# Kernel tuning notes

Measured on AMD Instinct MI355X. Metric: run time of the kernel, lower is better.

Reference implementation:

```python
import jax, jax.numpy as jnp
import numpy as np

B, X, Y, Z = 2, 64, 64, 48
T_IN, T_OUT = 10, 20
WIDTH = 20
G = 4              # number of fields / groups
M1 = M2 = M3 = 8   # fourier modes
L = 4              # layers
ORDER = [[0, 1, 2, 3], [1, 2, 3, 0], [2, 3, 0, 1], [3, 0, 1, 2]]
CIN = WIDTH * 4    # mWidth_input_parameters[i] == 4
COUT = WIDTH       # nWidth_output_parameters[i] == 1
EPS = 1e-5


def setup_inputs() -> dict:
    key = jax.random.key(0)
    ks = jax.random.split(key, 12)
    s = 0.02
    return {
        "x": jax.random.normal(ks[0], (B, X, Y, Z, G * T_IN), jnp.float32),
        "p_w": jax.random.normal(ks[1], (G, T_IN + 3, WIDTH), jnp.float32) * s,
        "p_b": jnp.zeros((G, WIDTH), jnp.float32),
        # complex spectral weights stored as (..., 2) = (real, imag); 4 corner blocks
        "spec_w": jax.random.normal(ks[2], (L, G, 4, CIN, COUT, M1, M2, M3, 2), jnp.float32) * (1.0 / CIN),
        "mlp_w1": jax.random.normal(ks[3], (L, G, COUT, COUT), jnp.float32) * s,
        "mlp_b1": jnp.zeros((L, G, COUT), jnp.float32),
        "mlp_w2": jax.random.normal(ks[4], (L, G, COUT, COUT), jnp.float32) * s,
        "mlp_b2": jnp.zeros((L, G, COUT), jnp.float32),
        "w_w": jax.random.normal(ks[5], (L, G, COUT, CIN), jnp.float32) * s,
        "w_b": jnp.zeros((L, G, COUT), jnp.float32),
        "q_w1": jax.random.normal(ks[6], (G, 4 * COUT, COUT), jnp.float32) * s,
        "q_b1": jnp.zeros((G, 4 * COUT), jnp.float32),
        "q_w2": jax.random.normal(ks[7], (G, T_OUT, 4 * COUT), jnp.float32) * s,
        "q_b2": jnp.zeros((G, T_OUT), jnp.float32),
    }


def _instance_norm(v):  # (B,C,X,Y,Z); InstanceNorm3d, affine=False
    m = v.mean(axis=(-3, -2, -1), keepdims=True)
    var = v.var(axis=(-3, -2, -1), keepdims=True)
    return (v - m) * jax.lax.rsqrt(var + EPS)


def _conv1x1(v, w, b):  # w: (Co, Ci)
    return jnp.einsum('bixyz,oi->boxyz', v, w) + b[None, :, None, None, None]


def _gelu(v):
    return jax.nn.gelu(v, approximate=False)


def _spectral(v, w):  # v: (B,Ci,X,Y,Z); w: complex (4,Ci,Co,M1,M2,M3)
    ft = jnp.fft.rfftn(v, axes=(-3, -2, -1))
    mul = lambda xc, wc: jnp.einsum('bixyz,ioxyz->boxyz', xc, wc)
    out = jnp.zeros((v.shape[0], w.shape[2], X, Y, Z // 2 + 1), ft.dtype)
    out = out.at[:, :, :M1, :M2, :M3].set(mul(ft[:, :, :M1, :M2, :M3], w[0]))
    out = out.at[:, :, -M1:, :M2, :M3].set(mul(ft[:, :, -M1:, :M2, :M3], w[1]))
    out = out.at[:, :, :M1, -M2:, :M3].set(mul(ft[:, :, :M1, -M2:, :M3], w[2]))
    out = out.at[:, :, -M1:, -M2:, :M3].set(mul(ft[:, :, -M1:, -M2:, :M3], w[3]))
    return jnp.fft.irfftn(out, s=(X, Y, Z), axes=(-3, -2, -1))


def _grid():  # (1,X,Y,Z,3), linspace 0..1 per axis
    gx = jnp.linspace(0.0, 1.0, X, dtype=jnp.float32)[:, None, None]
    gy = jnp.linspace(0.0, 1.0, Y, dtype=jnp.float32)[None, :, None]
    gz = jnp.linspace(0.0, 1.0, Z, dtype=jnp.float32)[None, None, :]
    g = jnp.stack([jnp.broadcast_to(gx, (X, Y, Z)),
                   jnp.broadcast_to(gy, (X, Y, Z)),
                   jnp.broadcast_to(gz, (X, Y, Z))], axis=-1)
    return g[None]


def reference(x, p_w, p_b, spec_w, mlp_w1, mlp_b1, mlp_w2, mlp_b2,
              w_w, w_b, q_w1, q_b1, q_w2, q_b2):
    grid = jnp.broadcast_to(_grid(), (x.shape[0], X, Y, Z, 3))
    # --- lifting: per-field Linear(T_in+3 -> width) ---
    lifted = [jnp.concatenate([x[..., i * T_IN:(i + 1) * T_IN], grid], axis=-1) @ p_w[i] + p_b[i]
              for i in range(G)]
    h = jnp.concatenate(lifted, axis=-1).transpose(0, 4, 1, 2, 3)  # (B, width*G, X, Y, Z)
    sw = spec_w[..., 0] + 1j * spec_w[..., 1]
    for l in range(L):
        for i in range(G):
            # faithful gather quirk: first index duplicated, last index dropped
            idx = [ORDER[i][0]] + ORDER[i][:-1]
            xg = jnp.concatenate([h[:, WIDTH * k:WIDTH * (k + 1)] for k in idx], axis=1)
            v = _instance_norm(xg)
            v = _spectral(v, sw[l, i])
            v = _instance_norm(v)
            v = _conv1x1(_gelu(_conv1x1(v, mlp_w1[l, i], mlp_b1[l, i])), mlp_w2[l, i], mlp_b2[l, i])
            r = _conv1x1(xg, w_w[l, i], w_b[l, i])
            h = h.at[:, WIDTH * i:WIDTH * (i + 1)].set(v + r)
        if l != L - 1:
            h = _gelu(h)
    # --- projection: per-field MLP (T_OUT == WIDTH so slices align to field blocks) ---
    outs = []
    for i in range(G):
        lo = (WIDTH if i == 0 else T_OUT) * i
        xi = h[:, lo:lo + WIDTH]
        xi = _conv1x1(_gelu(_conv1x1(xi, q_w1[i], q_b1[i])), q_w2[i], q_b2[i])
        outs.append(xi)
    out = jnp.concatenate(outs, axis=1)
    return out.transpose(0, 2, 3, 4, 1)  # (B,X,Y,Z,G*T_OUT)
```

## Files before the change

kernel.cpp:

```cpp
#include <hip/hip_runtime.h>
#include <math.h>

#define SPAT 196608
#define EPSV 1e-5f

__device__ __forceinline__ float geluf(float x){
    float ax = fabsf(x)*0.70710678118654752440f;
    float t = __builtin_amdgcn_rcpf(1.0f + 0.3275911f*ax);
    float p = ((((1.061405429f*t - 1.453152027f)*t + 1.421413741f)*t - 0.284496736f)*t + 0.254829592f)*t;
    float e = 1.0f - p*__expf(-ax*ax);
    float er = copysignf(e, x);
    return 0.5f*x*(1.0f + er);
}
__device__ __forceinline__ float wred(float v){
    #pragma unroll
    for(int o=32;o>0;o>>=1) v += __shfl_down(v,o);
    return v;
}

__global__ void k_tables(float* tab){
    for(int idx=threadIdx.x; idx<384; idx+=blockDim.x){
        int z = idx>>3, k = idx&7;
        double a = 6.283185307179586476925286766559 * (double)((k*z)%48) / 48.0;
        float c = (float)cos(a), s = (float)sin(a);
        tab[idx]=c; tab[384+idx]=s;
        tab[768 + k*48+z]=c; tab[1152 + k*48+z]=s;
    }
    for(int idx=threadIdx.x; idx<1024; idx+=blockDim.x){
        int y = idx>>4, ki = idx&15;
        int ka = ki<8 ? ki : ki+48;
        double a = 6.283185307179586476925286766559 * (double)((ka*y)%64) / 64.0;
        float c=(float)cos(a), s=(float)sin(a);
        tab[1536+idx]=c; tab[2560+idx]=s;
        tab[3584 + ki*64+y]=c; tab[4608 + ki*64+y]=s;
    }
}

__global__ void __launch_bounds__(256) k_lift(const float* __restrict__ x,
                       const float* __restrict__ pw, const float* __restrict__ pb,
                       float* __restrict__ h){
    int t = blockIdx.x*256 + threadIdx.x;
    int b = (t>=SPAT) ? 1 : 0; int col = t - b*SPAT;
    int xy = col/48, z = col%48;
    const float4* xp = (const float4*)(x + (size_t)t*40);
    float in[40];
    #pragma unroll
    for(int q=0;q<10;q++){
        float4 v = xp[q];
        in[q*4]=v.x; in[q*4+1]=v.y; in[q*4+2]=v.z; in[q*4+3]=v.w;
    }
    float gx = (float)(xy>>6)*(1.0f/63.0f);
    float gy = (float)(xy&63)*(1.0f/63.0f);
    float gz = (float)z*(1.0f/47.0f);
    for(int g=0;g<4;g++){
        const float* w = pw + g*260;
        #pragma unroll 4
        for(int c=0;c<20;c++){
            float a = pb[g*20+c];
            #pragma unroll
            for(int j=0;j<10;j++) a += in[g*10+j]*w[j*20+c];
            a += gx*w[200+c] + gy*w[220+c] + gz*w[240+c];
            h[(size_t)(b*80+g*20+c)*SPAT + col] = a;
        }
    }
}

__global__ void __launch_bounds__(256) k_zy(const float* __restrict__ h,
        float* __restrict__ ybuf, float* __restrict__ partZY,
        const float* __restrict__ tab, int gA,int gB,int gC,int gD, int gflag){
    __shared__ float sp4[4*16*65];
    __shared__ float cyl[16*65], syl[16*65];
    __shared__ float sred[8];
    __shared__ float comb[256];
    int blk = blockIdx.x;
    int x = blk&63; int d=(blk>>6)%20; int r2 = blk/1280; int b = r2&1; int gi = r2>>1;
    int gl4[4]={gA,gB,gC,gD};
    int g = gl4[gi];
    int ch = g*20+d;
    int tid=threadIdx.x;
    int y = tid&63, q4 = tid>>6;
    const float4* src = (const float4*)(h + (size_t)(b*80+ch)*SPAT + (size_t)x*3072
                                          + (size_t)(y*48 + q4*12));
    float v[12];
    #pragma unroll
    for(int u=0;u<3;u++){
        float4 t4 = src[u];
        v[u*4]=t4.x; v[u*4+1]=t4.y; v[u*4+2]=t4.z; v[u*4+3]=t4.w;
    }
    if(gflag){
        #pragma unroll
        for(int j=0;j<12;j++) v[j]=geluf(v[j]);
    }
    float s1=0,s2=0;
    #pragma unroll
    for(int j=0;j<12;j++){ s1+=v[j]; s2+=v[j]*v[j]; }
    for(int tt=tid;tt<1024;tt+=256){
        int ki=tt>>6, yy=tt&63;
        cyl[ki*65+yy]=tab[3584+tt]; syl[ki*65+yy]=tab[4608+tt];
    }
    const float* CZ = tab+768  + q4*12;
    const float* SZ = tab+1152 + q4*12;
    #pragma unroll
    for(int k=0;k<8;k++){
        float rr=0, si=0;
        #pragma unroll
        for(int j=0;j<12;j++){ rr += v[j]*CZ[k*48+j]; si += v[j]*SZ[k*48+j]; }
        sp4[(q4*16 + k*2)*65 + y]   = rr;
        sp4[(q4*16 + k*2+1)*65 + y] = -si;
    }
    s1=wred(s1); s2=wred(s2);
    if((tid&63)==0){ sred[(tid>>6)*2]=s1; sred[(tid>>6)*2+1]=s2; }
    __syncthreads();
    if(tid==0){
        size_t pi = ((size_t)(b*80+ch)*64+x)*2;
        partZY[pi]   = sred[0]+sred[2]+sred[4]+sred[6];
        partZY[pi+1] = sred[1]+sred[3]+sred[5]+sred[7];
    }
    #pragma unroll
    for(int j=0;j<4;j++){
        int e = tid + j*256;
        int kri = e>>6, yy = e&63;
        float sum = sp4[kri*65+yy] + sp4[(16+kri)*65+yy]
                  + sp4[(32+kri)*65+yy] + sp4[(48+kri)*65+yy];
        sp4[kri*65+yy] = sum;
    }
    __syncthreads();
    {
        int task = tid & 127;
        int half = tid >> 7;
        int ky = task>>3, kz = task&7;
        const float* cy  = cyl + ky*65 + half*32;
        const float* sy  = syl + ky*65 + half*32;
        const float* spr = sp4 + (kz*2)*65 + half*32;
        const float* spi = sp4 + (kz*2+1)*65 + half*32;
        float fr=0, fi=0;
        #pragma unroll 8
        for(int yy=0;yy<32;yy++){
            float sr=spr[yy], si=spi[yy];
            float c=cy[yy], s=sy[yy];
            fr += sr*c + si*s;
            fi += si*c - sr*s;
        }
        if(half){ comb[task*2]=fr; comb[task*2+1]=fi; }
        __syncthreads();
        if(!half){
            fr += comb[task*2]; fi += comb[task*2+1];
            size_t base = ((size_t)((g*2+b)*20+d)*16 + ky)*1024 + (size_t)(kz*128);
            ybuf[base + x]      = fr;
            ybuf[base + 64 + x] = fi;
        }
    }
}

__global__ void __launch_bounds__(128) k_xdft(const float* __restrict__ ybuf,
        float* __restrict__ fbufC, const float* __restrict__ partZY,
        const float* __restrict__ tab, int gA,int gB,int gC,int gD){
    __shared__ __align__(16) float ylx[16*68];
    __shared__ float cxl[16*65], sxl[16*65];
    __shared__ float scs[1];
    int blk = blockIdx.x;
    int kyi = blk&15; int d=(blk>>4)%20; int r2=blk/320; int b=r2&1; int gi=r2>>1;
    int gl4[4]={gA,gB,gC,gD};
    int g=gl4[gi]; int ch=g*20+d;
    int tid=threadIdx.x;
    const float4* src = (const float4*)(ybuf + (((size_t)((g*2+b)*20+d)*16+kyi)*1024));
    #pragma unroll
    for(int u=0;u<2;u++){
        int e=tid+u*128; float4 v=src[e];
        int kzri = e>>4; int xx=(e&15)*4;
        *(float4*)(ylx + kzri*68 + xx) = v;
    }
    for(int tt=tid;tt<1024;tt+=128){
        int ki=tt>>6, y=tt&63;
        cxl[ki*65+y]=tab[3584+tt]; sxl[ki*65+y]=tab[4608+tt];
    }
    float s1=0,s2=0;
    if(tid<64){
        size_t pi=((size_t)(b*80+ch)*64+tid)*2;
        s1=partZY[pi]; s2=partZY[pi+1];
    }
    s1=wred(s1); s2=wred(s2);
    if(tid==0){
        float mean=s1*(1.0f/196608.0f);
        float var=s2*(1.0f/196608.0f)-mean*mean;
        scs[0]=rsqrtf(var+EPSV);
    }
    __syncthreads();
    float sc = scs[0];
    int kxi=tid>>3, kz=tid&7;
    const float* yr = ylx + (kz*2)*68;
    const float* yi = ylx + (kz*2+1)*68;
    const float* cx = cxl + kxi*65;
    const float* sx = sxl + kxi*65;
    float fr=0, fi=0;
    #pragma unroll 8
    for(int xx=0;xx<64;xx++){
        float a=yr[xx], e2=yi[xx];
        float c=cx[xx], s=sx[xx];
        fr += a*c + e2*s;
        fi += e2*c - a*s;
    }
    fr*=sc; fi*=sc;
    if(kxi==0 && kyi==0 && kz==0){ fr=0.0f; fi=0.0f; }
    size_t idx = ((size_t)(b*80+ch)*2048 + (size_t)((kxi*16+kyi)*8+kz))*2;
    fbufC[idx]=fr; fbufC[idx+1]=fi;
}

__global__ void __launch_bounds__(256) k_spec2(const float* __restrict__ fbufC,
        const float* __restrict__ sw, float* __restrict__ gbuf,
        float* __restrict__ stat2, int li0,
        int i0, int gA1, int gA2, int i1, int gB1, int gB2){
    __shared__ float part[2112];
    int blk = blockIdx.x;
    int it = blk/320; int r = blk - it*320;
    int m1p = r & 3, o = (r>>2)%20, q = r/80;
    int li = li0 + it;
    int g0 = it ? i1 : i0;
    int g1 = it ? gB1 : gA1;
    int g2 = it ? gB2 : gA2;
    int tid = threadIdx.x;
    int t64 = tid & 63, cc = tid >> 6;
    if(q==0 && m1p==0 && tid<2){
        stat2[((it*2+tid)*20+o)*2]=0.f; stat2[((it*2+tid)*20+o)*2+1]=0.f;
    }
    int offx = (q&1)*8, offy = (q>>1)*8;
    int m1 = m1p*2 + (t64>>5);
    int m2 = (t64>>2)&7;
    int m3 = (t64&3)*2;
    int tw = m1*64 + m2*8 + m3;
    int kxi = m1+offx, kyi = m2+offy;
    int fo = (kxi*16 + kyi)*8 + m3;
    const float4* wp = (const float4*)(sw + (((size_t)(li*4+q)*1600) + o)*1024 + (size_t)tw*2);
    const float4* fb = (const float4*)fbufC + (fo>>1);
    float r00=0,i00=0,r01=0,i01=0, r10=0,i10=0,r11=0,i11=0;
    int c0 = cc*5;
    #pragma unroll
    for(int u=0;u<5;u++){
        int c = c0+u;
        float4 wa = wp[(size_t)c*5120];
        float4 wb4= wp[(size_t)(c+20)*5120];
        float wr0 = wa.x + wb4.x, wi0 = wa.y + wb4.y, wr1 = wa.z + wb4.z, wi1 = wa.w + wb4.w;
        float4 f0 = fb[(size_t)(g0*20+c)*1024];
        float4 f1 = fb[(size_t)(80+g0*20+c)*1024];
        r00 += f0.x*wr0 - f0.y*wi0; i00 += f0.x*wi0 + f0.y*wr0;
        r01 += f0.z*wr1 - f0.w*wi1; i01 += f0.z*wi1 + f0.w*wr1;
        r10 += f1.x*wr0 - f1.y*wi0; i10 += f1.x*wi0 + f1.y*wr0;
        r11 += f1.z*wr1 - f1.w*wi1; i11 += f1.z*wi1 + f1.w*wr1;
    }
    #pragma unroll
    for(int u=0;u<5;u++){
        int c = c0+u;
        float4 wa = wp[(size_t)(c+40)*5120];
        float4 f0 = fb[(size_t)(g1*20+c)*1024];
        float4 f1 = fb[(size_t)(80+g1*20+c)*1024];
        r00 += f0.x*wa.x - f0.y*wa.y; i00 += f0.x*wa.y + f0.y*wa.x;
        r01 += f0.z*wa.z - f0.w*wa.w; i01 += f0.z*wa.w + f0.w*wa.z;
        r10 += f1.x*wa.x - f1.y*wa.y; i10 += f1.x*wa.y + f1.y*wa.x;
        r11 += f1.z*wa.z - f1.w*wa.w; i11 += f1.z*wa.w + f1.w*wa.z;
    }
    #pragma unroll
    for(int u=0;u<5;u++){
        int c = c0+u;
        float4 wa = wp[(size_t)(c+60)*5120];
        float4 f0 = fb[(size_t)(g2*20+c)*1024];
        float4 f1 = fb[(size_t)(80+g2*20+c)*1024];
        r00 += f0.x*wa.x - f0.y*wa.y; i00 += f0.x*wa.y + f0.y*wa.x;
        r01 += f0.z*wa.z - f0.w*wa.w; i01 += f0.z*wa.w + f0.w*wa.z;
        r10 += f1.x*wa.x - f1.y*wa.y; i10 += f1.x*wa.y + f1.y*wa.x;
        r11 += f1.z*wa.z - f1.w*wa.w; i11 += f1.z*wa.w + f1.w*wa.z;
    }
    float vals[8]={r00,i00,r01,i01,r10,i10,r11,i11};
    #pragma unroll
    for(int e=0;e<8;e++) part[t64*33 + e*4 + cc] = vals[e];
    __syncthreads();
    if(cc==0){
        float acc[8];
        #pragma unroll
        for(int e=0;e<8;e++){
            const float* p = part + t64*33 + e*4;
            acc[e] = p[0]+p[1]+p[2]+p[3];
        }
        float* gb = gbuf + (size_t)it*163840;
        float4* gg0 = (float4*)(gb + (size_t)o*4096 + fo*2);
        float4* gg1 = (float4*)(gb + (size_t)(20+o)*4096 + fo*2);
        *gg0 = make_float4(acc[0],acc[1],acc[2],acc[3]);
        *gg1 = make_float4(acc[4],acc[5],acc[6],acc[7]);
    }
}

__global__ void k_inv2(const float* __restrict__ gbuf, float* __restrict__ iybuf,
                       float* __restrict__ stat2, const float* __restrict__ tab){
    __shared__ float gl[4224];
    __shared__ float tmp[256];
    __shared__ float cl[1088], sl[1088];
    __shared__ float ig[4];
    int blk = blockIdx.x;
    int it = blk/2560; int r = blk - it*2560;
    int nx = r&63, o = (r>>6)%20, b = r/1280;
    const float* srcf = gbuf + (size_t)it*163840 + (size_t)(b*20+o)*4096;
    for(int t=threadIdx.x;t<4096;t+=blockDim.x) gl[t + (t>>5)] = srcf[t];
    for(int t=threadIdx.x;t<1024;t+=blockDim.x){
        int y=t>>4, ki=t&15;
        cl[y*17+ki]=tab[1536+t]; sl[y*17+ki]=tab[2560+t];
    }
    __syncthreads();
    {
        int kyi = threadIdx.x>>3, kz = threadIdx.x&7;
        float ar=0, ai=0;
        #pragma unroll 4
        for(int kxi=0;kxi<16;kxi++){
            int v = ((kxi*16+kyi)*8+kz)*2;
            int pv = v + (v>>5);
            float gr = gl[pv], gi2 = gl[pv+1];
            float c = cl[nx*17+kxi], s = sl[nx*17+kxi];
            ar += gr*c - gi2*s;
            ai += gi2*c + gr*s;
        }
        tmp[threadIdx.x*2]   = ar*(1.0f/64.0f);
        tmp[threadIdx.x*2+1] = ai*(1.0f/64.0f);
    }
    __syncthreads();
    float p1=0,p2=0;
    for(int j=0;j<4;j++){
        int out = threadIdx.x + j*128;
        int ny = out>>3, kz = out&7;
        float ar=0, ai=0;
        #pragma unroll 4
        for(int kyi=0;kyi<16;kyi++){
            float vr = tmp[(kyi*8+kz)*2], vi = tmp[(kyi*8+kz)*2+1];
            float c = cl[ny*17+kyi], s = sl[ny*17+kyi];
            ar += vr*c - vi*s;
            ai += vi*c + vr*s;
        }
        ar *= (1.0f/64.0f); ai *= (1.0f/64.0f);
        size_t idx = ((((size_t)((it*2+b)*20+o)*64+nx)*64+ny)*8+kz)*2;
        iybuf[idx]=ar; iybuf[idx+1]=ai;
        if(kz==0){ p1 += ar; p2 += ar*ar; }
        else p2 += 2.0f*(ar*ar+ai*ai);
    }
    p2 *= (1.0f/48.0f);
    float r1=wred(p1), r2=wred(p2);
    int wv = threadIdx.x>>6;
    if((threadIdx.x&63)==0){ ig[wv*2]=r1; ig[wv*2+1]=r2; }
    __syncthreads();
    if(threadIdx.x==0){
        atomicAdd(&stat2[((it*2+b)*20+o)*2],   ig[0]+ig[2]);
        atomicAdd(&stat2[((it*2+b)*20+o)*2+1], ig[1]+ig[3]);
    }
}

__global__ void __launch_bounds__(192) k_passD2(
        const float* __restrict__ iybuf,
        const float* __restrict__ w1, const float* __restrict__ b1,
        const float* __restrict__ w2, const float* __restrict__ b2,
        const float* __restrict__ ww, const float* __restrict__ wb,
        float* __restrict__ h,
        const float* __restrict__ stat2, const float* __restrict__ tab,
        int li0, int i0, int i1, int gA1, int gA2, int gB1, int gB2,
        int fA0,int fA1,int fA2, int fB0,int fB1,int fB2){
    __shared__ __align__(16) float dl[5120];
    __shared__ float m2l[2][20], s2l[2][20];
    __shared__ float czl[384], szl[384];
    int blk = blockIdx.x;
    int nyt = blk&7, nx=(blk>>3)&63, b = blk>>9;
    int tid = threadIdx.x;
    for(int u=tid; u<1280; u+=192){
        int itu = (u>=640)?1:0; int rem = u - itu*640;
        int o = rem>>5, j = rem&31;
        const float4* s4 = (const float4*)(iybuf +
            ((((size_t)((itu*2+b)*20+o)*64+nx)*64 + nyt*8)*16));
        ((float4*)dl)[itu*640 + o*32 + j] = s4[j];
    }
    if(tid<40){
        int itq = tid/20, oq = tid - itq*20;
        float S1 = stat2[((itq*2+b)*20+oq)*2], S2 = stat2[((itq*2+b)*20+oq)*2+1];
        float mean = S1*(1.0f/196608.0f);
        float var = S2*(1.0f/196608.0f) - mean*mean;
        m2l[itq][oq]=mean; s2l[itq][oq]=rsqrtf(var+EPSV);
    }
    for(int t=tid;t<384;t+=192){ czl[t]=tab[768+t]; szl[t]=tab[1152+t]; }
    __syncthreads();
    int p0 = tid*2;
    int nyl = p0/48, nz0 = p0 - nyl*48;
    int sb = (nx*64 + nyt*8)*48;
    const float* hb = h + (size_t)(b*80)*SPAT + sb + p0;
    {
        float vj0[20], vj1[20];
        #pragma unroll
        for(int o=0;o<20;o++){
            const float* dd = dl + o*128 + nyl*16;
            float a0 = dd[0], a1 = dd[0];
            #pragma unroll
            for(int k=1;k<8;k++){
                float dr = dd[k*2], di = dd[k*2+1];
                a0 += 2.0f*(dr*czl[k*48+nz0]   - di*szl[k*48+nz0]);
                a1 += 2.0f*(dr*czl[k*48+nz0+1] - di*szl[k*48+nz0+1]);
            }
            vj0[o] = (a0*(1.0f/48.0f) - m2l[0][o])*s2l[0][o];
            vj1[o] = (a1*(1.0f/48.0f) - m2l[0][o])*s2l[0][o];
        }
        const float* W1 = w1 + li0*400; const float* W2 = w2 + li0*400;
        const float* B1 = b1 + li0*20;  const float* B2 = b2 + li0*20;
        float t10[20], t11[20];
        #pragma unroll
        for(int oo=0;oo<20;oo++){
            float a0=B1[oo], a1=a0;
            #pragma unroll
            for(int j=0;j<20;j++){ float w=W1[oo*20+j]; a0+=vj0[j]*w; a1+=vj1[j]*w; }
            t10[oo]=geluf(a0); t11[oo]=geluf(a1);
        }
        float o0[20], o1[20];
        #pragma unroll
        for(int oo=0;oo<20;oo++){
            float bb = B2[oo] + wb[li0*20+oo];
            float a0=bb, a1=bb;
            #pragma unroll
            for(int j=0;j<20;j++){ float w=W2[oo*20+j]; a0+=t10[j]*w; a1+=t11[j]*w; }
            o0[oo]=a0; o1[oo]=a1;
        }
        const float* W = ww + li0*1600;
        for(int c=0;c<20;c++){
            float2 vv = *(const float2*)(hb + (size_t)(i0*20+c)*SPAT);
            if(fA0){ vv.x=geluf(vv.x); vv.y=geluf(vv.y); }
            #pragma unroll
            for(int o=0;o<20;o++){
                float w = W[o*80+c] + W[o*80+20+c];
                o0[o]+=w*vv.x; o1[o]+=w*vv.y;
            }
        }
        for(int c=0;c<20;c++){
            float2 vv = *(const float2*)(hb + (size_t)(gA1*20+c)*SPAT);
            if(fA1){ vv.x=geluf(vv.x); vv.y=geluf(vv.y); }
            #pragma unroll
            for(int o=0;o<20;o++){
                float w = W[o*80+40+c];
                o0[o]+=w*vv.x; o1[o]+=w*vv.y;
            }
        }
        for(int c=0;c<20;c++){
            float2 vv = *(const float2*)(hb + (size_t)(gA2*20+c)*SPAT);
            if(fA2){ vv.x=geluf(vv.x); vv.y=geluf(vv.y); }
            #pragma unroll
            for(int o=0;o<20;o++){
                float w = W[o*80+60+c];
                o0[o]+=w*vv.x; o1[o]+=w*vv.y;
            }
        }
        #pragma unroll
        for(int o=0;o<20;o++)
            *(float2*)(h + (size_t)(b*80+i0*20+o)*SPAT + sb + p0) = make_float2(o0[o],o1[o]);
    }
    {
        int li1 = li0+1;
        float vj0[20], vj1[20];
        #pragma unroll
        for(int o=0;o<20;o++){
            const float* dd = dl + 2560 + o*128 + nyl*16;
            float a0 = dd[0], a1 = dd[0];
            #pragma unroll
            for(int k=1;k<8;k++){
                float dr = dd[k*2], di = dd[k*2+1];
                a0 += 2.0f*(dr*czl[k*48+nz0]   - di*szl[k*48+nz0]);
                a1 += 2.0f*(dr*czl[k*48+nz0+1] - di*szl[k*48+nz0+1]);
            }
            vj0[o] = (a0*(1.0f/48.0f) - m2l[1][o])*s2l[1][o];
            vj1[o] = (a1*(1.0f/48.0f) - m2l[1][o])*s2l[1][o];
        }
        const float* W1 = w1 + li1*400; const float* W2 = w2 + li1*400;
        const float* B1 = b1 + li1*20;  const float* B2 = b2 + li1*20;
        float t10[20], t11[20];
        #pragma unroll
        for(int oo=0;oo<20;oo++){
            float a0=B1[oo], a1=a0;
            #pragma unroll
            for(int j=0;j<20;j++){ float w=W1[oo*20+j]; a0+=vj0[j]*w; a1+=vj1[j]*w; }
            t10[oo]=geluf(a0); t11[oo]=geluf(a1);
        }
        float o0[20], o1[20];
        #pragma unroll
        for(int oo=0;oo<20;oo++){
            float bb = B2[oo] + wb[li1*20+oo];
            float a0=bb, a1=bb;
            #pragma unroll
            for(int j=0;j<20;j++){ float w=W2[oo*20+j]; a0+=t10[j]*w; a1+=t11[j]*w; }
            o0[oo]=a0; o1[oo]=a1;
        }
        const float* W = ww + li1*1600;
        for(int c=0;c<20;c++){
            float2 vv = *(const float2*)(hb + (size_t)(i1*20+c)*SPAT);
            if(fB0){ vv.x=geluf(vv.x); vv.y=geluf(vv.y); }
            #pragma unroll
            for(int o=0;o<20;o++){
                float w = W[o*80+c] + W[o*80+20+c];
                o0[o]+=w*vv.x; o1[o]+=w*vv.y;
            }
        }
        for(int c=0;c<20;c++){
            float2 vv = *(const float2*)(hb + (size_t)(gB1*20+c)*SPAT);
            if(fB1){ vv.x=geluf(vv.x); vv.y=geluf(vv.y); }
            #pragma unroll
            for(int o=0;o<20;o++){
                float w = W[o*80+40+c];
                o0[o]+=w*vv.x; o1[o]+=w*vv.y;
            }
        }
        for(int c=0;c<20;c++){
            float2 vv = *(const float2*)(hb + (size_t)(gB2*20+c)*SPAT);
            if(fB2){ vv.x=geluf(vv.x); vv.y=geluf(vv.y); }
            #pragma unroll
            for(int o=0;o<20;o++){
                float w = W[o*80+60+c];
                o0[o]+=w*vv.x; o1[o]+=w*vv.y;
            }
        }
        #pragma unroll
        for(int o=0;o<20;o++)
            *(float2*)(h + (size_t)(b*80+i1*20+o)*SPAT + sb + p0) = make_float2(o0[o],o1[o]);
    }
}

__global__ void __launch_bounds__(256) k_head(const float* __restrict__ h,
        const float* __restrict__ qw1, const float* __restrict__ qb1,
        const float* __restrict__ qw2, const float* __restrict__ qb2,
        float* __restrict__ out){
    int g = blockIdx.x & 3;
    int t = (blockIdx.x>>2)*256 + threadIdx.x;
    if(t >= 196608) return;
    int b = (t>=98304) ? 1 : 0; int col = (t - b*98304)*2;
    const float* hb = h + (size_t)(b*80+g*20)*SPAT + col;
    float2 in20[20];
    #pragma unroll
    for(int j=0;j<20;j++) in20[j] = *(const float2*)(hb + (size_t)j*SPAT);
    float2 o20[20];
    #pragma unroll
    for(int o2=0;o2<20;o2++){ float bv = qb2[g*20+o2]; o20[o2].x=bv; o20[o2].y=bv; }
    for(int o8=0;o8<80;o8++){
        float bv = qb1[g*80+o8];
        float a0=bv, a1=bv, c0=0.0f, c1=0.0f;
        #pragma unroll
        for(int j=0;j<10;j++){
            float w = qw1[g*1600 + o8*20 + j];
            a0 += in20[j].x*w; a1 += in20[j].y*w;
        }
        #pragma unroll
        for(int j=10;j<20;j++){
            float w = qw1[g*1600 + o8*20 + j];
            c0 += in20[j].x*w; c1 += in20[j].y*w;
        }
        a0 = geluf(a0+c0); a1 = geluf(a1+c1);
        #pragma unroll
        for(int o2=0;o2<20;o2++){
            float w = qw2[g*1600 + o2*80 + o8];
            o20[o2].x += a0*w; o20[o2].y += a1*w;
        }
    }
    float* op0 = out + ((size_t)(b*SPAT)+col)*80 + g*20;
    float* op1 = op0 + 80;
    #pragma unroll
    for(int q2=0;q2<5;q2++){
        *(float4*)(op0 + q2*4) = make_float4(o20[q2*4].x,o20[q2*4+1].x,o20[q2*4+2].x,o20[q2*4+3].x);
        *(float4*)(op1 + q2*4) = make_float4(o20[q2*4].y,o20[q2*4+1].y,o20[q2*4+2].y,o20[q2*4+3].y);
    }
}

extern "C" void kernel_launch(void* const* d_in, const int* in_sizes, int n_in,
                              void* d_out, int out_size, void* d_ws, size_t ws_size,
                              hipStream_t stream){
    (void)in_sizes; (void)n_in; (void)out_size;
    const float* x    = (const float*)d_in[0];
    const float* p_w  = (const float*)d_in[1];
    const float* p_b  = (const float*)d_in[2];
    const float* spec = (const float*)d_in[3];
    const float* w1   = (const float*)d_in[4];
    const float* b1   = (const float*)d_in[5];
    const float* w2   = (const float*)d_in[6];
    const float* b2   = (const float*)d_in[7];
    const float* ww   = (const float*)d_in[8];
    const float* wb   = (const float*)d_in[9];
    const float* qw1  = (const float*)d_in[10];
    const float* qb1  = (const float*)d_in[11];
    const float* qw2  = (const float*)d_in[12];
    const float* qb2  = (const float*)d_in[13];
    float* out = (float*)d_out;
    float* ws  = (float*)d_ws;

    if(ws_size < (size_t)40330912*4) return;

    float* h      = ws;
    float* ybuf   = ws + 31457280;
    float* gbuf   = ws + 34078720;
    float* iyb    = ws + 34406400;
    float* fbufC  = ws + 39649280;
    float* partZY = ws + 40304640;
    float* stat2  = ws + 40325120;
    float* tab    = ws + 40325280;

    k_tables<<<1,256,0,stream>>>(tab);
    k_lift<<<1536,256,0,stream>>>(x, p_w, p_b, h);

    static const int ORD3[4][3] = {{0,1,2},{1,2,3},{2,3,0},{3,0,1}};
    for(int l=0;l<4;l++){
        int lf = (l>0)?1:0;
        for(int bi=0;bi<2;bi++){
            if(bi==0){
                k_zy  <<<10240,256,0,stream>>>(h, ybuf, partZY, tab, 0,1,2,3, lf);
                k_xdft<<< 2560,128,0,stream>>>(ybuf, fbufC, partZY, tab, 0,1,2,3);
            } else {
                k_zy  <<< 5120,256,0,stream>>>(h, ybuf, partZY, tab, 0,1,0,0, 0);
                k_xdft<<< 1280,128,0,stream>>>(ybuf, fbufC, partZY, tab, 0,1,0,0);
            }
            int i0 = bi*2, i1 = i0+1, li0 = l*4+i0;
            int gA1=ORD3[i0][1], gA2=ORD3[i0][2];
            int gB1=ORD3[i1][1], gB2=ORD3[i1][2];
            k_spec2<<< 640,256,0,stream>>>(fbufC, spec, gbuf, stat2, li0,
                                           i0,gA1,gA2, i1,gB1,gB2);
            k_inv2 <<<5120,128,0,stream>>>(gbuf, iyb, stat2, tab);
            int fA0 = lf;
            int fA1 = (gA1<i0)?0:lf;
            int fA2 = (gA2<i0)?0:lf;
            int fB0 = lf;
            int fB1 = (gB1<i1)?0:lf;
            int fB2 = (gB2<i1)?0:lf;
            k_passD2<<<1024,192,0,stream>>>(iyb, w1,b1,w2,b2, ww,wb, h, stat2, tab,
                                            li0, i0,i1, gA1,gA2, gB1,gB2,
                                            fA0,fA1,fA2, fB0,fB1,fB2);
        }
    }
    k_head<<<3072,256,0,stream>>>(h, qw1, qb1, qw2, qb2, out);
}
```

Before: 3.122 ms.

## Fuse z/y and x forward DFT kernels into a single per-channel kernel

Merges the z/y partial-DFT kernel and the x-DFT kernel into one k_fwd kernel, with one block per (group, batch, channel). Each block loops over all x slabs, keeps the intermediate y-spectrum in LDS and computes the instance-norm statistics locally. This removes the ybuf and partZY global round trips and one launch per stage. In exchange, the grid drops to 80–160 large blocks with heavy LDS and register use, which likely underfills the GPU and hides memory latency poorly. Separately, k_passD2 now launches 256 threads to speed up the cooperative loads, and the extra threads exit before compute.

```diff
diff --git a/kernel.cpp b/kernel.cpp
--- a/kernel.cpp
+++ b/kernel.cpp
@@ -65,145 +65,111 @@
     }
 }
 
-__global__ void __launch_bounds__(256) k_zy(const float* __restrict__ h,
-        float* __restrict__ ybuf, float* __restrict__ partZY,
-        const float* __restrict__ tab, int gA,int gB,int gC,int gD, int gflag){
-    __shared__ float sp4[4*16*65];
-    __shared__ float cyl[16*65], syl[16*65];
+__global__ void __launch_bounds__(256) k_fwd(const float* __restrict__ h,
+        float* __restrict__ fbufC, const float* __restrict__ tab,
+        int gA,int gB,int gC,int gD, int gflag){
+    __shared__ float zls[4*1040];
+    __shared__ float cylp[16*130];
+    __shared__ float ylds[128*130];
     __shared__ float sred[8];
-    __shared__ float comb[256];
+    __shared__ float scs[1];
     int blk = blockIdx.x;
-    int x = blk&63; int d=(blk>>6)%20; int r2 = blk/1280; int b = r2&1; int gi = r2>>1;
+    int d = blk%20; int b = (blk/20)&1; int gi = blk/40;
     int gl4[4]={gA,gB,gC,gD};
-    int g = gl4[gi];
-    int ch = g*20+d;
-    int tid=threadIdx.x;
-    int y = tid&63, q4 = tid>>6;
-    const float4* src = (const float4*)(h + (size_t)(b*80+ch)*SPAT + (size_t)x*3072
-                                          + (size_t)(y*48 + q4*12));
-    float v[12];
-    #pragma unroll
-    for(int u=0;u<3;u++){
-        float4 t4 = src[u];
-        v[u*4]=t4.x; v[u*4+1]=t4.y; v[u*4+2]=t4.z; v[u*4+3]=t4.w;
-    }
-    if(gflag){
-        #pragma unroll
-        for(int j=0;j<12;j++) v[j]=geluf(v[j]);
-    }
-    float s1=0,s2=0;
-    #pragma unroll
-    for(int j=0;j<12;j++){ s1+=v[j]; s2+=v[j]*v[j]; }
+    int ch = gl4[gi]*20 + d;
+    int tid = threadIdx.x;
     for(int tt=tid;tt<1024;tt+=256){
         int ki=tt>>6, yy=tt&63;
-        cyl[ki*65+yy]=tab[3584+tt]; syl[ki*65+yy]=tab[4608+tt];
-    }
-    const float* CZ = tab+768  + q4*12;
-    const float* SZ = tab+1152 + q4*12;
-    #pragma unroll
-    for(int k=0;k<8;k++){
-        float rr=0, si=0;
-        #pragma unroll
-        for(int j=0;j<12;j++){ rr += v[j]*CZ[k*48+j]; si += v[j]*SZ[k*48+j]; }
-        sp4[(q4*16 + k*2)*65 + y]   = rr;
-        sp4[(q4*16 + k*2+1)*65 + y] = -si;
+        cylp[ki*130+yy*2]   = tab[3584+tt];
+        cylp[ki*130+yy*2+1] = tab[4608+tt];
+    }
+    int y = tid&63, xsub = tid>>6;
+    const float* hc = h + (size_t)(b*80+ch)*SPAT;
+    const float* CZ = tab+768;
+    const float* SZ = tab+1152;
+    float s1=0, s2=0;
+    for(int xc=0;xc<16;xc++){
+        int x = xc*4 + xsub;
+        float v[48];
+        const float4* src = (const float4*)(hc + (size_t)x*3072 + y*48);
+        #pragma unroll
+        for(int u=0;u<12;u++){
+            float4 t4 = src[u];
+            v[u*4]=t4.x; v[u*4+1]=t4.y; v[u*4+2]=t4.z; v[u*4+3]=t4.w;
+        }
+        if(gflag){
+            #pragma unroll
+            for(int j=0;j<48;j++) v[j]=geluf(v[j]);
+        }
+        #pragma unroll
+        for(int j=0;j<48;j++){ s1+=v[j]; s2+=v[j]*v[j]; }
+        float zr[8], zi[8];
+        #pragma unroll
+        for(int k=0;k<8;k++){
+            float rr=0, si=0;
+            #pragma unroll
+            for(int j=0;j<48;j++){ rr += v[j]*CZ[k*48+j]; si += v[j]*SZ[k*48+j]; }
+            zr[k]=rr; zi[k]=-si;
+        }
+        __syncthreads();
+        #pragma unroll
+        for(int k=0;k<8;k++)
+            *(float2*)(zls + xsub*1040 + k*130 + y*2) = make_float2(zr[k], zi[k]);
+        __syncthreads();
+        int task = tid & 127;
+        int ky = task>>3, kz = task&7;
+        #pragma unroll
+        for(int i2=0;i2<2;i2++){
+            int xs = (tid>>7)*2 + i2;
+            const float* sp = zls + xs*1040 + kz*130;
+            const float* cy = cylp + ky*130;
+            float fr=0, fi=0;
+            #pragma unroll 8
+            for(int yy=0;yy<64;yy++){
+                float2 sv = *(const float2*)(sp + yy*2);
+                float2 cs = *(const float2*)(cy + yy*2);
+                fr += sv.x*cs.x + sv.y*cs.y;
+                fi += sv.y*cs.x - sv.x*cs.y;
+            }
+            *(float2*)(ylds + task*130 + (xc*4+xs)*2) = make_float2(fr, fi);
+        }
     }
     s1=wred(s1); s2=wred(s2);
     if((tid&63)==0){ sred[(tid>>6)*2]=s1; sred[(tid>>6)*2+1]=s2; }
     __syncthreads();
     if(tid==0){
-        size_t pi = ((size_t)(b*80+ch)*64+x)*2;
-        partZY[pi]   = sred[0]+sred[2]+sred[4]+sred[6];
-        partZY[pi+1] = sred[1]+sred[3]+sred[5]+sred[7];
-    }
-    #pragma unroll
-    for(int j=0;j<4;j++){
-        int e = tid + j*256;
-        int kri = e>>6, yy = e&63;
-        float sum = sp4[kri*65+yy] + sp4[(16+kri)*65+yy]
-                  + sp4[(32+kri)*65+yy] + sp4[(48+kri)*65+yy];
-        sp4[kri*65+yy] = sum;
-    }
-    __syncthreads();
-    {
-        int task = tid & 127;
-        int half = tid >> 7;
-        int ky = task>>3, kz = task&7;
-        const float* cy  = cyl + ky*65 + half*32;
-        const float* sy  = syl + ky*65 + half*32;
-        const float* spr = sp4 + (kz*2)*65 + half*32;
-        const float* spi = sp4 + (kz*2+1)*65 + half*32;
-        float fr=0, fi=0;
-        #pragma unroll 8
-        for(int yy=0;yy<32;yy++){
-            float sr=spr[yy], si=spi[yy];
-            float c=cy[yy], s=sy[yy];
-            fr += sr*c + si*s;
-            fi += si*c - sr*s;
-        }
-        if(half){ comb[task*2]=fr; comb[task*2+1]=fi; }
-        __syncthreads();
-        if(!half){
-            fr += comb[task*2]; fi += comb[task*2+1];
-            size_t base = ((size_t)((g*2+b)*20+d)*16 + ky)*1024 + (size_t)(kz*128);
-            ybuf[base + x]      = fr;
-            ybuf[base + 64 + x] = fi;
-        }
-    }
-}
-
-__global__ void __launch_bounds__(128) k_xdft(const float* __restrict__ ybuf,
-        float* __restrict__ fbufC, const float* __restrict__ partZY,
-        const float* __restrict__ tab, int gA,int gB,int gC,int gD){
-    __shared__ __align__(16) float ylx[16*68];
-    __shared__ float cxl[16*65], sxl[16*65];
-    __shared__ float scs[1];
-    int blk = blockIdx.x;
-    int kyi = blk&15; int d=(blk>>4)%20; int r2=blk/320; int b=r2&1; int gi=r2>>1;
-    int gl4[4]={gA,gB,gC,gD};
-    int g=gl4[gi]; int ch=g*20+d;
-    int tid=threadIdx.x;
-    const float4* src = (const float4*)(ybuf + (((size_t)((g*2+b)*20+d)*16+kyi)*1024));
-    #pragma unroll
-    for(int u=0;u<2;u++){
-        int e=tid+u*128; float4 v=src[e];
-        int kzri = e>>4; int xx=(e&15)*4;
-        *(float4*)(ylx + kzri*68 + xx) = v;
-    }
-    for(int tt=tid;tt<1024;tt+=128){
-        int ki=tt>>6, y=tt&63;
-        cxl[ki*65+y]=tab[3584+tt]; sxl[ki*65+y]=tab[4608+tt];
-    }
-    float s1=0,s2=0;
-    if(tid<64){
-        size_t pi=((size_t)(b*80+ch)*64+tid)*2;
-        s1=partZY[pi]; s2=partZY[pi+1];
-    }
-    s1=wred(s1); s2=wred(s2);
-    if(tid==0){
-        float mean=s1*(1.0f/196608.0f);
-        float var=s2*(1.0f/196608.0f)-mean*mean;
-        scs[0]=rsqrtf(var+EPSV);
+        float S1 = sred[0]+sred[2]+sred[4]+sred[6];
+        float S2 = sred[1]+sred[3]+sred[5]+sred[7];
+        float mean = S1*(1.0f/196608.0f);
+        float var = S2*(1.0f/196608.0f) - mean*mean;
+        scs[0] = rsqrtf(var + EPSV);
     }
     __syncthreads();
     float sc = scs[0];
-    int kxi=tid>>3, kz=tid&7;
-    const float* yr = ylx + (kz*2)*68;
-    const float* yi = ylx + (kz*2+1)*68;
-    const float* cx = cxl + kxi*65;
-    const float* sx = sxl + kxi*65;
-    float fr=0, fi=0;
-    #pragma unroll 8
-    for(int xx=0;xx<64;xx++){
-        float a=yr[xx], e2=yi[xx];
-        float c=cx[xx], s=sx[xx];
-        fr += a*c + e2*s;
-        fi += e2*c - a*s;
-    }
-    fr*=sc; fi*=sc;
-    if(kxi==0 && kyi==0 && kz==0){ fr=0.0f; fi=0.0f; }
-    size_t idx = ((size_t)(b*80+ch)*2048 + (size_t)((kxi*16+kyi)*8+kz))*2;
-    fbufC[idx]=fr; fbufC[idx+1]=fi;
+    int task = tid&127, kxih = tid>>7;
+    int kyi = task>>3, kz = task&7;
+    float ar[8], ai[8];
+    #pragma unroll
+    for(int k8=0;k8<8;k8++){ ar[k8]=0.0f; ai[k8]=0.0f; }
+    const float* row = ylds + task*130;
+    for(int x=0;x<64;x++){
+        float2 vv = *(const float2*)(row + x*2);
+        #pragma unroll
+        for(int k8=0;k8<8;k8++){
+            float2 cs = *(const float2*)(cylp + (kxih*8+k8)*130 + x*2);
+            ar[k8] += vv.x*cs.x + vv.y*cs.y;
+            ai[k8] += vv.y*cs.x - vv.x*cs.y;
+        }
+    }
+    float* fc = fbufC + (size_t)(b*80+ch)*4096;
+    #pragma unroll
+    for(int k8=0;k8<8;k8++){
+        int kxi = kxih*8+k8;
+        float fr = ar[k8]*sc, fi = ai[k8]*sc;
+        if(kxi==0 && kyi==0 && kz==0){ fr=0.0f; fi=0.0f; }
+        size_t idx = (size_t)((kxi*16+kyi)*8+kz)*2;
+        fc[idx]=fr; fc[idx+1]=fi;
+    }
 }
 
 __global__ void __launch_bounds__(256) k_spec2(const float* __restrict__ fbufC,
@@ -349,7 +315,7 @@
     }
 }
 
-__global__ void __launch_bounds__(192) k_passD2(
+__global__ void __launch_bounds__(256) k_passD2(
         const float* __restrict__ iybuf,
         const float* __restrict__ w1, const float* __restrict__ b1,
         const float* __restrict__ w2, const float* __restrict__ b2,
@@ -364,7 +330,7 @@
     int blk = blockIdx.x;
     int nyt = blk&7, nx=(blk>>3)&63, b = blk>>9;
     int tid = threadIdx.x;
-    for(int u=tid; u<1280; u+=192){
+    for(int u=tid; u<1280; u+=256){
         int itu = (u>=640)?1:0; int rem = u - itu*640;
         int o = rem>>5, j = rem&31;
         const float4* s4 = (const float4*)(iybuf +
@@ -378,8 +344,9 @@
         float var = S2*(1.0f/196608.0f) - mean*mean;
         m2l[itq][oq]=mean; s2l[itq][oq]=rsqrtf(var+EPSV);
     }
-    for(int t=tid;t<384;t+=192){ czl[t]=tab[768+t]; szl[t]=tab[1152+t]; }
-    __syncthreads();
+    for(int t=tid;t<384;t+=256){ czl[t]=tab[768+t]; szl[t]=tab[1152+t]; }
+    __syncthreads();
+    if(tid>=192) return;
     int p0 = tid*2;
     int nyl = p0/48, nz0 = p0 - nyl*48;
     int sb = (nx*64 + nyt*8)*48;
@@ -584,16 +551,14 @@
     float* out = (float*)d_out;
     float* ws  = (float*)d_ws;
 
-    if(ws_size < (size_t)40330912*4) return;
+    if(ws_size < (size_t)37689008*4) return;
 
     float* h      = ws;
-    float* ybuf   = ws + 31457280;
-    float* gbuf   = ws + 34078720;
-    float* iyb    = ws + 34406400;
-    float* fbufC  = ws + 39649280;
-    float* partZY = ws + 40304640;
-    float* stat2  = ws + 40325120;
-    float* tab    = ws + 40325280;
+    float* gbuf   = ws + 31457280;
+    float* iyb    = ws + 31784960;
+    float* fbufC  = ws + 37027840;
+    float* stat2  = ws + 37683200;
+    float* tab    = ws + 37683360;
 
     k_tables<<<1,256,0,stream>>>(tab);
     k_lift<<<1536,256,0,stream>>>(x, p_w, p_b, h);
@@ -603,11 +568,9 @@
         int lf = (l>0)?1:0;
         for(int bi=0;bi<2;bi++){
             if(bi==0){
-                k_zy  <<<10240,256,0,stream>>>(h, ybuf, partZY, tab, 0,1,2,3, lf);
-                k_xdft<<< 2560,128,0,stream>>>(ybuf, fbufC, partZY, tab, 0,1,2,3);
+                k_fwd<<<160,256,0,stream>>>(h, fbufC, tab, 0,1,2,3, lf);
             } else {
-                k_zy  <<< 5120,256,0,stream>>>(h, ybuf, partZY, tab, 0,1,0,0, 0);
-                k_xdft<<< 1280,128,0,stream>>>(ybuf, fbufC, partZY, tab, 0,1,0,0);
+                k_fwd<<< 80,256,0,stream>>>(h, fbufC, tab, 0,1,0,0, 0);
             }
             int i0 = bi*2, i1 = i0+1, li0 = l*4+i0;
             int gA1=ORD3[i0][1], gA2=ORD3[i0][2];
@@ -621,7 +584,7 @@
             int fB0 = lf;
             int fB1 = (gB1<i1)?0:lf;
             int fB2 = (gB2<i1)?0:lf;
-            k_passD2<<<1024,192,0,stream>>>(iyb, w1,b1,w2,b2, ww,wb, h, stat2, tab,
+            k_passD2<<<1024,256,0,stream>>>(iyb, w1,b1,w2,b2, ww,wb, h, stat2, tab,
                                             li0, i0,i1, gA1,gA2, gB1,gB2,
                                             fA0,fA1,fA2, fB0,fB1,fB2);
         }
```

New measurement: 3.809 ms. 1.22x slower.
